# Kernel tuning notes

Hardware: AMD Instinct MI355X
Metric: run time of the kernel (lower is better)

## Reference

```python
import jax, jax.numpy as jnp
import numpy as np

T, B = 256, 64
NTOKEN, NINP, NHID = 256, 64, 4096


def setup_inputs() -> dict:
    key = jax.random.key(0)
    k1, k2, k3, k4, k5, k6, k7 = jax.random.split(key, 7)
    tokens = jax.random.randint(k1, (T, B), 0, NTOKEN)            # [T, B] byte ids
    seq_len = jax.random.randint(k2, (B,), 1, T + 1)              # per-sample valid length in [1, T]
    s_in = 1.0 / np.sqrt(NINP)
    s_h = 1.0 / np.sqrt(NHID)
    emb_table = jax.random.normal(k3, (NTOKEN, NINP), jnp.float32)
    w_ih = jax.random.normal(k4, (4 * NHID, NINP), jnp.float32) * s_in
    w_hh = jax.random.normal(k5, (4 * NHID, NHID), jnp.float32) * s_h
    b_ih = jax.random.normal(k6, (4 * NHID,), jnp.float32) * s_h
    b_hh = jax.random.normal(k7, (4 * NHID,), jnp.float32) * s_h
    return {"tokens": tokens, "seq_len": seq_len, "emb_table": emb_table,
            "w_ih": w_ih, "w_hh": w_hh, "b_ih": b_ih, "b_hh": b_hh}


def reference(tokens, seq_len, emb_table, w_ih, w_hh, b_ih, b_hh):
    # Embedding lookup for all timesteps (dropout p=0.0 -> identity).
    emb = emb_table[tokens]                                   # [T, B, ninp]
    # Precompute input projections for every step (batched GEMM).
    x_proj = jnp.einsum('tbi,gi->tbg', emb, w_ih) + b_ih + b_hh  # [T, B, 4H]
    H = w_hh.shape[1]
    h0 = jnp.zeros((tokens.shape[1], H), x_proj.dtype)
    c0 = jnp.zeros_like(h0)
    feat0 = jnp.zeros_like(h0)

    def step(carry, inp):
        h, c, feat = carry
        xp, t = inp
        gates = xp + h @ w_hh.T                               # [B, 4H]
        i_g, f_g, g_g, o_g = jnp.split(gates, 4, axis=-1)     # torch gate order i,f,g,o
        c = jax.nn.sigmoid(f_g) * c + jax.nn.sigmoid(i_g) * jnp.tanh(g_g)
        h = jax.nn.sigmoid(o_g) * jnp.tanh(c)
        # get_valid_outs: at step t>0, keep previous feature once t >= seq_len.
        valid = (t < seq_len) | (t == 0)                      # [B]
        feat = jnp.where(valid[:, None], c, feat)
        return (h, c, feat), None

    (_, _, feat), _ = jax.lax.scan(step, (h0, c0, feat0),
                                   (x_proj, jnp.arange(x_proj.shape[0])))
    return feat                                               # [B, nhid]
```

## Files before the change

kernel.cpp:

```cpp
#include <hip/hip_runtime.h>
#include <hip/hip_bf16.h>

#define TSTEPS 256
#define BATCH  64
#define NINP   64
#define NHID   4096
#define NGATE  (4 * NHID)
#define KDIM   (NINP + NHID)
#define NCHUNK (KDIM / 32)
#define NGRP   (NGATE / 16)

typedef __bf16 bf16x8 __attribute__((ext_vector_type(8)));
typedef float  f32x4  __attribute__((ext_vector_type(4)));
typedef unsigned short ushort_t;

__device__ __forceinline__ ushort_t f2b(float v) {
    __hip_bfloat16 h = __float2bfloat16(v);
    return *reinterpret_cast<ushort_t*>(&h);
}
__device__ __forceinline__ float sigf(float x) { return 1.f / (1.f + expf(-x)); }


__global__ void k_convert(const float* __restrict__ w_ih, const float* __restrict__ w_hh,
                          const float* __restrict__ b_ih, const float* __restrict__ b_hh,
                          ushort_t* __restrict__ Wp, float* __restrict__ bias) {
    const int grp = blockIdx.x;
    for (int i = threadIdx.x; i < 16 * KDIM; i += 256) {
        int r = i / KDIM;
        int k = i - r * KDIM;
        int g = grp * 16 + r;
        float v = (k < NINP) ? w_ih[(size_t)g * NINP + k]
                             : w_hh[(size_t)g * NHID + (k - NINP)];
        int c = k >> 5, q = (k >> 3) & 3, e = k & 7;
        Wp[((size_t)grp * NCHUNK + c) * 512 + (q * 16 + r) * 8 + e] = f2b(v);
    }
    if (threadIdx.x < 16) {
        int g = grp * 16 + threadIdx.x;
        bias[g] = b_ih[g] + b_hh[g];
    }
}

__global__ void k_init(const int* __restrict__ tokens, const float* __restrict__ emb,
                       ushort_t* __restrict__ A0, float* __restrict__ cbuf) {
    int idx = blockIdx.x * 256 + threadIdx.x;
    if (idx < BATCH * KDIM) {
        int b = idx / KDIM, k = idx - b * KDIM;
        float v = (k < NINP) ? emb[tokens[b] * NINP + k] : 0.f;
        int c = k >> 5, q = (k >> 3) & 3, e = k & 7;
        A0[((size_t)(b >> 4) * NCHUNK + c) * 512 + (q * 16 + (b & 15)) * 8 + e] = f2b(v);
    }
    if (idx < BATCH * NHID) cbuf[idx] = 0.f;
}

__global__ __launch_bounds__(512)
void k_step(int t, const ushort_t* __restrict__ Wp, const float* __restrict__ bias,
            const ushort_t* __restrict__ Ac, ushort_t* __restrict__ An,
            float* __restrict__ cbuf, float* __restrict__ out,
            const int* __restrict__ tokens, const int* __restrict__ seq_len,
            const float* __restrict__ emb) {
    const int tid  = threadIdx.x;
    const int wave = tid >> 6;
    const int lane = tid & 63;
    const int bx   = blockIdx.x;
    const int j0   = bx * 16;

    __shared__ float sbuf[BATCH][66];

    for (int i = tid; i < BATCH * 66; i += 512)
        (&sbuf[0][0])[i] = 0.f;

    if (bx == 0 && (t + 1) < TSTEPS) {
        for (int i = tid; i < BATCH * NINP; i += 512) {
            int b = i >> 6, k = i & 63;
            int tok = tokens[(t + 1) * BATCH + b];
            float v = emb[tok * NINP + k];
            int c = k >> 5, q = (k >> 3) & 3, e = k & 7;
            An[((size_t)(b >> 4) * NCHUNK + c) * 512 + (q * 16 + (b & 15)) * 8 + e] = f2b(v);
        }
    }
    __syncthreads();

    const int cstart = wave * 16 + (wave < 2 ? wave : 2);
    const int cend   = cstart + (wave < 2 ? 17 : 16);

    const ushort_t* pw0 = Wp + ((size_t)(0 * 256 + bx) * NCHUNK) * 512 + lane * 8;
    const ushort_t* pw1 = Wp + ((size_t)(1 * 256 + bx) * NCHUNK) * 512 + lane * 8;
    const ushort_t* pw2 = Wp + ((size_t)(2 * 256 + bx) * NCHUNK) * 512 + lane * 8;
    const ushort_t* pw3 = Wp + ((size_t)(3 * 256 + bx) * NCHUNK) * 512 + lane * 8;
    const ushort_t* pa0 = Ac + ((size_t)0 * NCHUNK) * 512 + lane * 8;
    const ushort_t* pa1 = Ac + ((size_t)1 * NCHUNK) * 512 + lane * 8;
    const ushort_t* pa2 = Ac + ((size_t)2 * NCHUNK) * 512 + lane * 8;
    const ushort_t* pa3 = Ac + ((size_t)3 * NCHUNK) * 512 + lane * 8;

    f32x4 acc[4][4];
    #pragma unroll
    for (int rt = 0; rt < 4; ++rt)
        #pragma unroll
        for (int gt = 0; gt < 4; ++gt)
            acc[rt][gt] = (f32x4){0.f, 0.f, 0.f, 0.f};

    #define LOADF(dstW, dstA, c)                                              \
        do {                                                                  \
            size_t off = (size_t)(c) * 512;                                   \
            dstW[0] = *reinterpret_cast<const bf16x8*>(pw0 + off);            \
            dstW[1] = *reinterpret_cast<const bf16x8*>(pw1 + off);            \
            dstW[2] = *reinterpret_cast<const bf16x8*>(pw2 + off);            \
            dstW[3] = *reinterpret_cast<const bf16x8*>(pw3 + off);            \
            dstA[0] = *reinterpret_cast<const bf16x8*>(pa0 + off);            \
            dstA[1] = *reinterpret_cast<const bf16x8*>(pa1 + off);            \
            dstA[2] = *reinterpret_cast<const bf16x8*>(pa2 + off);            \
            dstA[3] = *reinterpret_cast<const bf16x8*>(pa3 + off);            \
        } while (0)

    bf16x8 curW[4], curA[4], nxtW[4], nxtA[4];
    LOADF(curW, curA, cstart);

    for (int c = cstart; c < cend - 1; ++c) {
        LOADF(nxtW, nxtA, c + 1);
        #pragma unroll
        for (int rt = 0; rt < 4; ++rt)
            #pragma unroll
            for (int gt = 0; gt < 4; ++gt)
                acc[rt][gt] = __builtin_amdgcn_mfma_f32_16x16x32_bf16(
                    curA[rt], curW[gt], acc[rt][gt], 0, 0, 0);
        #pragma unroll
        for (int z = 0; z < 4; ++z) { curW[z] = nxtW[z]; curA[z] = nxtA[z]; }
    }
    #pragma unroll
    for (int rt = 0; rt < 4; ++rt)
        #pragma unroll
        for (int gt = 0; gt < 4; ++gt)
            acc[rt][gt] = __builtin_amdgcn_mfma_f32_16x16x32_bf16(
                curA[rt], curW[gt], acc[rt][gt], 0, 0, 0);
    #undef LOADF

    {
        const int n = lane & 15, q = lane >> 4;
        #pragma unroll
        for (int rt = 0; rt < 4; ++rt)
            #pragma unroll
            for (int gt = 0; gt < 4; ++gt)
                #pragma unroll
                for (int r = 0; r < 4; ++r)
                    atomicAdd(&sbuf[rt * 16 + q * 4 + r][gt * 16 + n], acc[rt][gt][r]);
    }
    __syncthreads();

    {
        const int b  = lane;
        const int sl = seq_len[b];
        const bool valid = (t < sl) || (t == 0);
        #pragma unroll
        for (int jj = 0; jj < 2; ++jj) {
            int jl = wave + jj * 8;
            int j  = j0 + jl;
            float ig = sbuf[b][ 0 + jl] + bias[          j];
            float fg = sbuf[b][16 + jl] + bias[    NHID + j];
            float gg = sbuf[b][32 + jl] + bias[2 * NHID + j];
            float og = sbuf[b][48 + jl] + bias[3 * NHID + j];
            int cidx = b * NHID + j;
            float cold = cbuf[cidx];
            float cn = sigf(fg) * cold + sigf(ig) * tanhf(gg);
            float hn = sigf(og) * tanhf(cn);
            cbuf[cidx] = cn;
            if (valid) out[cidx] = cn;
            int kk = NINP + j;
            int c = kk >> 5, q = (kk >> 3) & 3, e = kk & 7;
            An[((size_t)(b >> 4) * NCHUNK + c) * 512 + (q * 16 + (b & 15)) * 8 + e] = f2b(hn);
        }
    }
}

extern "C" void kernel_launch(void* const* d_in, const int* in_sizes, int n_in,
                              void* d_out, int out_size, void* d_ws, size_t ws_size,
                              hipStream_t stream) {
    const int*   tokens  = (const int*)d_in[0];
    const int*   seq_len = (const int*)d_in[1];
    const float* emb     = (const float*)d_in[2];
    const float* w_ih    = (const float*)d_in[3];
    const float* w_hh    = (const float*)d_in[4];
    const float* b_ih    = (const float*)d_in[5];
    const float* b_hh    = (const float*)d_in[6];
    float* out = (float*)d_out;

    char* ws = (char*)d_ws;
    const size_t W_BYTES    = (size_t)NGRP * NCHUNK * 512 * 2;
    const size_t BIAS_BYTES = (size_t)NGATE * 4;
    const size_t C_BYTES    = (size_t)BATCH * NHID * 4;
    const size_t A_BYTES    = (size_t)4 * NCHUNK * 512 * 2;

    ushort_t* Wp   = (ushort_t*)ws;
    float*    bias = (float*)(ws + W_BYTES);
    float*    cbuf = (float*)(ws + W_BYTES + BIAS_BYTES);
    ushort_t* A0   = (ushort_t*)(ws + W_BYTES + BIAS_BYTES + C_BYTES);
    ushort_t* A1   = (ushort_t*)(ws + W_BYTES + BIAS_BYTES + C_BYTES + A_BYTES);

    k_convert<<<NGRP, 256, 0, stream>>>(w_ih, w_hh, b_ih, b_hh, Wp, bias);

    int init_elems = BATCH * KDIM;
    k_init<<<(init_elems + 255) / 256, 256, 0, stream>>>(tokens, emb, A0, cbuf);

    for (int t = 0; t < TSTEPS; ++t) {
        ushort_t* Acur  = (t & 1) ? A1 : A0;
        ushort_t* Anext = (t & 1) ? A0 : A1;
        k_step<<<256, 512, 0, stream>>>(t, Wp, bias, Acur, Anext, cbuf, out,
                                        tokens, seq_len, emb);
    }
}
```

Measured before the change: 17.23 ms.

## Replace per-step kernel launches with persistent cooperative kernel and grid barrier

Replaces 256 separate step launches with one cooperative persistent kernel that loops over timesteps and synchronises all 256 blocks through an atomic counter/generation grid barrier. The cell state is kept in registers for the whole run instead of a global c buffer, and biases and output offsets are hoisted out of the time loop. The goal is to remove per-launch overhead and global c-state traffic. The cost is a spin barrier per step and reliance on all blocks being co-resident.

```diff
diff --git a/kernel.cpp b/kernel.cpp
--- a/kernel.cpp
+++ b/kernel.cpp
@@ -9,6 +9,7 @@
 #define KDIM   (NINP + NHID)
 #define NCHUNK (KDIM / 32)
 #define NGRP   (NGATE / 16)
+#define NBLK   256
 
 typedef __bf16 bf16x8 __attribute__((ext_vector_type(8)));
 typedef float  f32x4  __attribute__((ext_vector_type(4)));
@@ -41,7 +42,7 @@
 }
 
 __global__ void k_init(const int* __restrict__ tokens, const float* __restrict__ emb,
-                       ushort_t* __restrict__ A0, float* __restrict__ cbuf) {
+                       ushort_t* __restrict__ A0, int* __restrict__ sync) {
     int idx = blockIdx.x * 256 + threadIdx.x;
     if (idx < BATCH * KDIM) {
         int b = idx / KDIM, k = idx - b * KDIM;
@@ -49,36 +50,42 @@
         int c = k >> 5, q = (k >> 3) & 3, e = k & 7;
         A0[((size_t)(b >> 4) * NCHUNK + c) * 512 + (q * 16 + (b & 15)) * 8 + e] = f2b(v);
     }
-    if (idx < BATCH * NHID) cbuf[idx] = 0.f;
-}
-
-__global__ __launch_bounds__(512)
-void k_step(int t, const ushort_t* __restrict__ Wp, const float* __restrict__ bias,
-            const ushort_t* __restrict__ Ac, ushort_t* __restrict__ An,
-            float* __restrict__ cbuf, float* __restrict__ out,
-            const int* __restrict__ tokens, const int* __restrict__ seq_len,
-            const float* __restrict__ emb) {
+    if (idx < 2) sync[idx] = 0;
+}
+
+__global__ __launch_bounds__(512, 2)
+void k_persist(const ushort_t* __restrict__ Wp, const float* __restrict__ bias,
+               ushort_t* __restrict__ A0, ushort_t* __restrict__ A1,
+               float* __restrict__ out,
+               const int* __restrict__ tokens, const int* __restrict__ seq_len,
+               const float* __restrict__ emb, int* __restrict__ sync) {
     const int tid  = threadIdx.x;
     const int wave = tid >> 6;
     const int lane = tid & 63;
     const int bx   = blockIdx.x;
     const int j0   = bx * 16;
 
+    int* cnt = sync;
+    int* gen = sync + 1;
+
     __shared__ float sbuf[BATCH][66];
 
-    for (int i = tid; i < BATCH * 66; i += 512)
-        (&sbuf[0][0])[i] = 0.f;
-
-    if (bx == 0 && (t + 1) < TSTEPS) {
-        for (int i = tid; i < BATCH * NINP; i += 512) {
-            int b = i >> 6, k = i & 63;
-            int tok = tokens[(t + 1) * BATCH + b];
-            float v = emb[tok * NINP + k];
-            int c = k >> 5, q = (k >> 3) & 3, e = k & 7;
-            An[((size_t)(b >> 4) * NCHUNK + c) * 512 + (q * 16 + (b & 15)) * 8 + e] = f2b(v);
-        }
-    }
-    __syncthreads();
+    const int jA = j0 + wave, jB = j0 + wave + 8;
+    float cA = 0.f, cB = 0.f;
+    const int  slen  = seq_len[lane];
+    const float bAi = bias[jA],            bBi = bias[jB];
+    const float bAf = bias[NHID + jA],     bBf = bias[NHID + jB];
+    const float bAg = bias[2 * NHID + jA], bBg = bias[2 * NHID + jB];
+    const float bAo = bias[3 * NHID + jA], bBo = bias[3 * NHID + jB];
+    size_t hoffA, hoffB;
+    {
+        int kk = NINP + jA;
+        int c = kk >> 5, q = (kk >> 3) & 3, e = kk & 7;
+        hoffA = ((size_t)(lane >> 4) * NCHUNK + c) * 512 + (q * 16 + (lane & 15)) * 8 + e;
+        kk = NINP + jB;
+        c = kk >> 5; q = (kk >> 3) & 3; e = kk & 7;
+        hoffB = ((size_t)(lane >> 4) * NCHUNK + c) * 512 + (q * 16 + (lane & 15)) * 8 + e;
+    }
 
     const int cstart = wave * 16 + (wave < 2 ? wave : 2);
     const int cend   = cstart + (wave < 2 ? 17 : 16);
@@ -87,86 +94,130 @@
     const ushort_t* pw1 = Wp + ((size_t)(1 * 256 + bx) * NCHUNK) * 512 + lane * 8;
     const ushort_t* pw2 = Wp + ((size_t)(2 * 256 + bx) * NCHUNK) * 512 + lane * 8;
     const ushort_t* pw3 = Wp + ((size_t)(3 * 256 + bx) * NCHUNK) * 512 + lane * 8;
-    const ushort_t* pa0 = Ac + ((size_t)0 * NCHUNK) * 512 + lane * 8;
-    const ushort_t* pa1 = Ac + ((size_t)1 * NCHUNK) * 512 + lane * 8;
-    const ushort_t* pa2 = Ac + ((size_t)2 * NCHUNK) * 512 + lane * 8;
-    const ushort_t* pa3 = Ac + ((size_t)3 * NCHUNK) * 512 + lane * 8;
-
-    f32x4 acc[4][4];
-    #pragma unroll
-    for (int rt = 0; rt < 4; ++rt)
+
+    int lgen = 0;
+
+    for (int t = 0; t < TSTEPS; ++t) {
+        ushort_t* Ac = (t & 1) ? A1 : A0;
+        ushort_t* An = (t & 1) ? A0 : A1;
+
+        for (int i = tid; i < BATCH * 66; i += 512)
+            (&sbuf[0][0])[i] = 0.f;
+
+        const ushort_t* pa0 = Ac + ((size_t)0 * NCHUNK) * 512 + lane * 8;
+        const ushort_t* pa1 = Ac + ((size_t)1 * NCHUNK) * 512 + lane * 8;
+        const ushort_t* pa2 = Ac + ((size_t)2 * NCHUNK) * 512 + lane * 8;
+        const ushort_t* pa3 = Ac + ((size_t)3 * NCHUNK) * 512 + lane * 8;
+
+        f32x4 acc[4][4];
         #pragma unroll
-        for (int gt = 0; gt < 4; ++gt)
-            acc[rt][gt] = (f32x4){0.f, 0.f, 0.f, 0.f};
-
-    #define LOADF(dstW, dstA, c)                                              \
-        do {                                                                  \
-            size_t off = (size_t)(c) * 512;                                   \
-            dstW[0] = *reinterpret_cast<const bf16x8*>(pw0 + off);            \
-            dstW[1] = *reinterpret_cast<const bf16x8*>(pw1 + off);            \
-            dstW[2] = *reinterpret_cast<const bf16x8*>(pw2 + off);            \
-            dstW[3] = *reinterpret_cast<const bf16x8*>(pw3 + off);            \
-            dstA[0] = *reinterpret_cast<const bf16x8*>(pa0 + off);            \
-            dstA[1] = *reinterpret_cast<const bf16x8*>(pa1 + off);            \
-            dstA[2] = *reinterpret_cast<const bf16x8*>(pa2 + off);            \
-            dstA[3] = *reinterpret_cast<const bf16x8*>(pa3 + off);            \
-        } while (0)
-
-    bf16x8 curW[4], curA[4], nxtW[4], nxtA[4];
-    LOADF(curW, curA, cstart);
-
-    for (int c = cstart; c < cend - 1; ++c) {
-        LOADF(nxtW, nxtA, c + 1);
+        for (int rt = 0; rt < 4; ++rt)
+            #pragma unroll
+            for (int gt = 0; gt < 4; ++gt)
+                acc[rt][gt] = (f32x4){0.f, 0.f, 0.f, 0.f};
+
+        #define LOADF(dstW, dstA, c)                                          \
+            do {                                                              \
+                size_t off = (size_t)(c) * 512;                               \
+                dstW[0] = *reinterpret_cast<const bf16x8*>(pw0 + off);        \
+                dstW[1] = *reinterpret_cast<const bf16x8*>(pw1 + off);        \
+                dstW[2] = *reinterpret_cast<const bf16x8*>(pw2 + off);        \
+                dstW[3] = *reinterpret_cast<const bf16x8*>(pw3 + off);        \
+                dstA[0] = *reinterpret_cast<const bf16x8*>(pa0 + off);        \
+                dstA[1] = *reinterpret_cast<const bf16x8*>(pa1 + off);        \
+                dstA[2] = *reinterpret_cast<const bf16x8*>(pa2 + off);        \
+                dstA[3] = *reinterpret_cast<const bf16x8*>(pa3 + off);        \
+            } while (0)
+
+        bf16x8 curW[4], curA[4], nxtW[4], nxtA[4];
+        LOADF(curW, curA, cstart);
+
+        __syncthreads();
+
+        for (int c = cstart; c < cend - 1; ++c) {
+            LOADF(nxtW, nxtA, c + 1);
+            #pragma unroll
+            for (int rt = 0; rt < 4; ++rt)
+                #pragma unroll
+                for (int gt = 0; gt < 4; ++gt)
+                    acc[rt][gt] = __builtin_amdgcn_mfma_f32_16x16x32_bf16(
+                        curA[rt], curW[gt], acc[rt][gt], 0, 0, 0);
+            #pragma unroll
+            for (int z = 0; z < 4; ++z) { curW[z] = nxtW[z]; curA[z] = nxtA[z]; }
+        }
         #pragma unroll
         for (int rt = 0; rt < 4; ++rt)
             #pragma unroll
             for (int gt = 0; gt < 4; ++gt)
                 acc[rt][gt] = __builtin_amdgcn_mfma_f32_16x16x32_bf16(
                     curA[rt], curW[gt], acc[rt][gt], 0, 0, 0);
-        #pragma unroll
-        for (int z = 0; z < 4; ++z) { curW[z] = nxtW[z]; curA[z] = nxtA[z]; }
-    }
-    #pragma unroll
-    for (int rt = 0; rt < 4; ++rt)
-        #pragma unroll
-        for (int gt = 0; gt < 4; ++gt)
-            acc[rt][gt] = __builtin_amdgcn_mfma_f32_16x16x32_bf16(
-                curA[rt], curW[gt], acc[rt][gt], 0, 0, 0);
-    #undef LOADF
-
-    {
-        const int n = lane & 15, q = lane >> 4;
-        #pragma unroll
-        for (int rt = 0; rt < 4; ++rt)
-            #pragma unroll
-            for (int gt = 0; gt < 4; ++gt)
+        #undef LOADF
+
+        {
+            const int n = lane & 15, q = lane >> 4;
+            #pragma unroll
+            for (int rt = 0; rt < 4; ++rt)
                 #pragma unroll
-                for (int r = 0; r < 4; ++r)
-                    atomicAdd(&sbuf[rt * 16 + q * 4 + r][gt * 16 + n], acc[rt][gt][r]);
-    }
-    __syncthreads();
-
-    {
-        const int b  = lane;
-        const int sl = seq_len[b];
-        const bool valid = (t < sl) || (t == 0);
-        #pragma unroll
-        for (int jj = 0; jj < 2; ++jj) {
-            int jl = wave + jj * 8;
-            int j  = j0 + jl;
-            float ig = sbuf[b][ 0 + jl] + bias[          j];
-            float fg = sbuf[b][16 + jl] + bias[    NHID + j];
-            float gg = sbuf[b][32 + jl] + bias[2 * NHID + j];
-            float og = sbuf[b][48 + jl] + bias[3 * NHID + j];
-            int cidx = b * NHID + j;
-            float cold = cbuf[cidx];
-            float cn = sigf(fg) * cold + sigf(ig) * tanhf(gg);
-            float hn = sigf(og) * tanhf(cn);
-            cbuf[cidx] = cn;
-            if (valid) out[cidx] = cn;
-            int kk = NINP + j;
-            int c = kk >> 5, q = (kk >> 3) & 3, e = kk & 7;
-            An[((size_t)(b >> 4) * NCHUNK + c) * 512 + (q * 16 + (b & 15)) * 8 + e] = f2b(hn);
+                for (int gt = 0; gt < 4; ++gt)
+                    #pragma unroll
+                    for (int r = 0; r < 4; ++r)
+                        atomicAdd(&sbuf[rt * 16 + q * 4 + r][gt * 16 + n], acc[rt][gt][r]);
+        }
+        __syncthreads();
+
+        {
+            const int b = lane;
+            const bool valid = (t < slen) || (t == 0);
+            {
+                int jl = wave;
+                float ig = sbuf[b][ 0 + jl] + bAi;
+                float fg = sbuf[b][16 + jl] + bAf;
+                float gg = sbuf[b][32 + jl] + bAg;
+                float og = sbuf[b][48 + jl] + bAo;
+                cA = sigf(fg) * cA + sigf(ig) * tanhf(gg);
+                float hn = sigf(og) * tanhf(cA);
+                if (valid) out[b * NHID + jA] = cA;
+                An[hoffA] = f2b(hn);
+            }
+            {
+                int jl = wave + 8;
+                float ig = sbuf[b][ 0 + jl] + bBi;
+                float fg = sbuf[b][16 + jl] + bBf;
+                float gg = sbuf[b][32 + jl] + bBg;
+                float og = sbuf[b][48 + jl] + bBo;
+                cB = sigf(fg) * cB + sigf(ig) * tanhf(gg);
+                float hn = sigf(og) * tanhf(cB);
+                if (valid) out[b * NHID + jB] = cB;
+                An[hoffB] = f2b(hn);
+            }
+        }
+
+        if (bx == 0 && (t + 1) < TSTEPS) {
+            for (int i = tid; i < BATCH * NINP; i += 512) {
+                int b = i >> 6, k = i & 63;
+                int tok = tokens[(t + 1) * BATCH + b];
+                float v = emb[tok * NINP + k];
+                int c = k >> 5, q = (k >> 3) & 3, e = k & 7;
+                An[((size_t)(b >> 4) * NCHUNK + c) * 512 + (q * 16 + (b & 15)) * 8 + e] = f2b(v);
+            }
+        }
+
+        if (t + 1 < TSTEPS) {
+            __syncthreads();
+            if (tid == 0) {
+                __threadfence();
+                if (atomicAdd(cnt, 1) == NBLK - 1) {
+                    __hip_atomic_store(cnt, 0, __ATOMIC_RELAXED, __HIP_MEMORY_SCOPE_AGENT);
+                    __threadfence();
+                    __hip_atomic_store(gen, lgen + 1, __ATOMIC_RELEASE, __HIP_MEMORY_SCOPE_AGENT);
+                } else {
+                    while (__hip_atomic_load(gen, __ATOMIC_RELAXED, __HIP_MEMORY_SCOPE_AGENT) <= lgen)
+                        __builtin_amdgcn_s_sleep(1);
+                }
+                __threadfence();
+            }
+            __syncthreads();
+            ++lgen;
         }
     }
 }
@@ -186,24 +237,20 @@
     char* ws = (char*)d_ws;
     const size_t W_BYTES    = (size_t)NGRP * NCHUNK * 512 * 2;
     const size_t BIAS_BYTES = (size_t)NGATE * 4;
-    const size_t C_BYTES    = (size_t)BATCH * NHID * 4;
     const size_t A_BYTES    = (size_t)4 * NCHUNK * 512 * 2;
 
     ushort_t* Wp   = (ushort_t*)ws;
     float*    bias = (float*)(ws + W_BYTES);
-    float*    cbuf = (float*)(ws + W_BYTES + BIAS_BYTES);
-    ushort_t* A0   = (ushort_t*)(ws + W_BYTES + BIAS_BYTES + C_BYTES);
-    ushort_t* A1   = (ushort_t*)(ws + W_BYTES + BIAS_BYTES + C_BYTES + A_BYTES);
+    ushort_t* A0   = (ushort_t*)(ws + W_BYTES + BIAS_BYTES);
+    ushort_t* A1   = (ushort_t*)(ws + W_BYTES + BIAS_BYTES + A_BYTES);
+    int*      sync = (int*)(ws + W_BYTES + BIAS_BYTES + 2 * A_BYTES);
 
     k_convert<<<NGRP, 256, 0, stream>>>(w_ih, w_hh, b_ih, b_hh, Wp, bias);
 
     int init_elems = BATCH * KDIM;
-    k_init<<<(init_elems + 255) / 256, 256, 0, stream>>>(tokens, emb, A0, cbuf);
-
-    for (int t = 0; t < TSTEPS; ++t) {
-        ushort_t* Acur  = (t & 1) ? A1 : A0;
-        ushort_t* Anext = (t & 1) ? A0 : A1;
-        k_step<<<256, 512, 0, stream>>>(t, Wp, bias, Acur, Anext, cbuf, out,
-                                        tokens, seq_len, emb);
-    }
-}
+    k_init<<<(init_elems + 255) / 256, 256, 0, stream>>>(tokens, emb, A0, sync);
+
+    void* args[] = {(void*)&Wp, (void*)&bias, (void*)&A0, (void*)&A1, (void*)&out,
+                    (void*)&tokens, (void*)&seq_len, (void*)&emb, (void*)&sync};
+    hipLaunchCooperativeKernel((void*)k_persist, dim3(NBLK), dim3(512), args, 0, stream);
+}
```

New measurement: 25.54 ms. 48.2% more time.
